# Optimization experiments

Measured on AMD Instinct MI355X. Metric: run time of the kernel, lower is better.

The kernel has to match this reference:

```python
import jax, jax.numpy as jnp
import numpy as np

H = 256  # HIDDEN_SIZE
E = 256  # EMBED_SIZE
B = 128
L = 2048


def setup_inputs() -> dict:
    key = jax.random.key(0)
    ks = jax.random.split(key, 14)
    s = 1.0 / np.sqrt(H)
    return {
        "input_embed": jax.random.normal(ks[0], (B, 1, E), jnp.float32),
        "encoder_outputs": jax.random.normal(ks[1], (B, L, H), jnp.float32),
        "hidden1": jax.random.normal(ks[2], (1, B, H), jnp.float32),
        "cell1": jax.random.normal(ks[3], (1, B, H), jnp.float32),
        "hidden2": jax.random.normal(ks[4], (1, B, H), jnp.float32),
        "cell2": jax.random.normal(ks[5], (1, B, H), jnp.float32),
        "w_ih1": jax.random.normal(ks[6], (4 * H, H), jnp.float32) * s,
        "w_hh1": jax.random.normal(ks[7], (4 * H, H), jnp.float32) * s,
        "b_ih1": jax.random.normal(ks[8], (4 * H,), jnp.float32) * s,
        "b_hh1": jax.random.normal(ks[9], (4 * H,), jnp.float32) * s,
        "w_ih2": jax.random.normal(ks[10], (4 * H, E + H), jnp.float32) * s,
        "w_hh2": jax.random.normal(ks[11], (4 * H, H), jnp.float32) * s,
        "b_ih2": jax.random.normal(ks[12], (4 * H,), jnp.float32) * s,
        "b_hh2": jax.random.normal(ks[13], (4 * H,), jnp.float32) * s,
    }


def _lstm_step(x, h, c, w_ih, w_hh, b_ih, b_hh):
    # x: [B, D_in]; h, c: [B, H]. PyTorch gate order: i, f, g, o.
    gates = x @ w_ih.T + h @ w_hh.T + b_ih + b_hh  # [B, 4H]
    i, f, g, o = jnp.split(gates, 4, axis=-1)
    c_new = jax.nn.sigmoid(f) * c + jax.nn.sigmoid(i) * jnp.tanh(g)
    h_new = jax.nn.sigmoid(o) * jnp.tanh(c_new)
    return h_new, c_new


def reference(input_embed, encoder_outputs, hidden1, cell1, hidden2, cell2,
              w_ih1, w_hh1, b_ih1, b_hh1, w_ih2, w_hh2, b_ih2, b_hh2):
    # Attention: dot-product scores between hidden1[0] and each encoder step.
    scores = jnp.einsum('bh,blh->bl', hidden1[0], encoder_outputs)  # [B, L]
    alpha = jax.nn.softmax(scores, axis=1)
    context = jnp.einsum('bl,blh->bh', alpha, encoder_outputs)  # [B, H]

    # LSTM1 single step on the context vector.
    h1, c1 = _lstm_step(context, hidden1[0], cell1[0], w_ih1, w_hh1, b_ih1, b_hh1)
    mid = h1[:, None, :]  # [B, 1, H]

    # Concat embedding with LSTM1 output, run LSTM2 single step.
    new_mid = jnp.concatenate([input_embed[:, 0, :], h1], axis=-1)  # [B, E+H]
    h2, c2 = _lstm_step(new_mid, hidden2[0], cell2[0], w_ih2, w_hh2, b_ih2, b_hh2)
    outputs = h2[:, None, :]  # [B, 1, H]

    return (outputs, h1[None], c1[None], h2[None], c2[None])
```

## Files before the change

### kernel.cpp

```cpp
#include <hip/hip_runtime.h>
#include <math.h>

#define BN   128
#define LN   2048
#define HN   256
#define EN   256
#define CHUNKS 8
#define ROWS_PER_CHUNK (LN / CHUNKS)
#define PSTRIDE 260

__device__ __forceinline__ float sigmoidf_(float x) { return 1.0f / (1.0f + __expf(-x)); }
__device__ __forceinline__ float tanhf_(float x)    { return 1.0f - 2.0f / (__expf(2.0f * x) + 1.0f); }

__global__ __launch_bounds__(256) void attn_partial(
    const float* __restrict__ enc,
    const float* __restrict__ hidden1,
    float* __restrict__ partials)
{
    const int chunk = blockIdx.x;
    const int b     = blockIdx.y;
    const int t     = threadIdx.x;
    const int wave  = t >> 6;
    const int lane  = t & 63;

    __shared__ float lds_ctx[4][256];
    __shared__ float lds_m[4], lds_s[4];

    const float4 h4 = *(const float4*)(hidden1 + b * HN + lane * 4);

    float  m = -INFINITY, s = 0.0f;
    float4 ctx = make_float4(0.f, 0.f, 0.f, 0.f);

    const float* rowp = enc + ((size_t)b * LN + (size_t)chunk * ROWS_PER_CHUNK + wave * 64) * HN + lane * 4;

    #pragma unroll 2
    for (int r = 0; r < 64; ++r) {
        float4 e = *(const float4*)rowp;
        rowp += HN;
        float d = e.x * h4.x + e.y * h4.y + e.z * h4.z + e.w * h4.w;
        #pragma unroll
        for (int off = 32; off > 0; off >>= 1) d += __shfl_xor(d, off, 64);
        float mn   = fmaxf(m, d);
        float corr = __expf(m - mn);
        float p    = __expf(d - mn);
        s = s * corr + p;
        ctx.x = ctx.x * corr + p * e.x;
        ctx.y = ctx.y * corr + p * e.y;
        ctx.z = ctx.z * corr + p * e.z;
        ctx.w = ctx.w * corr + p * e.w;
        m = mn;
    }

    *(float4*)&lds_ctx[wave][lane * 4] = ctx;
    if (lane == 0) { lds_m[wave] = m; lds_s[wave] = s; }
    __syncthreads();

    float M = fmaxf(fmaxf(lds_m[0], lds_m[1]), fmaxf(lds_m[2], lds_m[3]));
    float e0 = __expf(lds_m[0] - M), e1 = __expf(lds_m[1] - M);
    float e2 = __expf(lds_m[2] - M), e3 = __expf(lds_m[3] - M);
    float cj = e0 * lds_ctx[0][t] + e1 * lds_ctx[1][t] + e2 * lds_ctx[2][t] + e3 * lds_ctx[3][t];
    float S  = e0 * lds_s[0] + e1 * lds_s[1] + e2 * lds_s[2] + e3 * lds_s[3];

    float* pb = partials + ((size_t)b * CHUNKS + chunk) * PSTRIDE;
    pb[t] = cj;
    if (t == 0) { pb[256] = M; pb[257] = S; }
}

#define STAGE_W1(Wp)                                                          \
    {                                                                         \
        _Pragma("unroll")                                                     \
        for (int it = 0; it < 16; ++it) {                                     \
            const int idx = it * 128 + t;                                     \
            const int row = idx & 31;                             \
            const int kf  = idx >> 5;               \
            const int q   = row >> 3, jl0 = row & 7;                          \
            const int g   = q * 256 + jb * 8 + jl0;                           \
            float4 v = *(const float4*)((Wp) + (size_t)g * 256 + kf * 4);     \
            const int pos = ((jl0 ^ (kf & 7)) << 2) + q;                      \
            wq[kf * 128 +  0 + pos] = v.x;                                    \
            wq[kf * 128 + 32 + pos] = v.y;                                    \
            wq[kf * 128 + 64 + pos] = v.z;                                    \
            wq[kf * 128 + 96 + pos] = v.w;                                    \
        }                                                                     \
    }

__global__ __launch_bounds__(128) void lstm1_fused(
    const float* __restrict__ partials,
    const float* __restrict__ hidden1,
    const float* __restrict__ w_ih,
    const float* __restrict__ w_hh,
    const float* __restrict__ b_ih,
    const float* __restrict__ b_hh,
    const float* __restrict__ cell,
    float* __restrict__ h_out,
    float* __restrict__ c_out)
{
    __shared__ float wq[256 * 32];
    __shared__ float xs[16 * 512];
    const int t  = threadIdx.x;
    const int jb = blockIdx.x;
    const int bb = blockIdx.y;

    STAGE_W1(w_ih);

    {
        const int g  = t >> 3;
        const int l8 = t & 7;
        const int b  = bb * 16 + g;
        const float* pb = partials + (size_t)b * CHUNKS * PSTRIDE;

        float mk[CHUNKS], ek[CHUNKS];
        float M = -INFINITY;
        #pragma unroll
        for (int k = 0; k < CHUNKS; ++k) { mk[k] = pb[k * PSTRIDE + 256]; M = fmaxf(M, mk[k]); }
        float S = 0.0f;
        #pragma unroll
        for (int k = 0; k < CHUNKS; ++k) { ek[k] = __expf(mk[k] - M); S += ek[k] * pb[k * PSTRIDE + 257]; }
        const float invS = 1.0f / S;

        #pragma unroll
        for (int it = 0; it < 8; ++it) {
            const int j4 = it * 8 + l8;
            float cx = 0.f, cy = 0.f, cz = 0.f, cw = 0.f;
            #pragma unroll
            for (int k = 0; k < CHUNKS; ++k) {
                float4 p4 = *(const float4*)(pb + k * PSTRIDE + j4 * 4);
                cx += ek[k] * p4.x; cy += ek[k] * p4.y;
                cz += ek[k] * p4.z; cw += ek[k] * p4.w;
            }
            *(float4*)&xs[g * 512 + ((j4 ^ (g & 7)) << 2)] =
                make_float4(cx * invS, cy * invS, cz * invS, cw * invS);
        }
        const float* hr = hidden1 + (size_t)b * HN;
        #pragma unroll
        for (int it = 0; it < 8; ++it) {
            const int j4 = it * 8 + l8;
            float4 hv = *(const float4*)(hr + j4 * 4);
            *(float4*)&xs[g * 512 + (((64 + j4) ^ (g & 7)) << 2)] = hv;
        }
    }
    __syncthreads();

    const int jl = t & 7, bl = t >> 3;
    const int b = bb * 16 + bl;
    const int j = jb * 8 + jl;

    float acc0 = 0.f, acc1 = 0.f, acc2 = 0.f, acc3 = 0.f;

    #pragma unroll 4
    for (int k4 = 0; k4 < 64; ++k4) {
        float4 xv = *(const float4*)&xs[bl * 512 + ((k4 ^ (bl & 7)) << 2)];
        const int pos = (jl ^ (k4 & 7)) << 2;
        #pragma unroll
        for (int i = 0; i < 4; ++i) {
            float xe = (i == 0) ? xv.x : (i == 1) ? xv.y : (i == 2) ? xv.z : xv.w;
            float4 w4 = *(const float4*)&wq[(k4 * 4 + i) * 32 + pos];
            acc0 += w4.x * xe; acc1 += w4.y * xe; acc2 += w4.z * xe; acc3 += w4.w * xe;
        }
    }
    __syncthreads();

    STAGE_W1(w_hh);
    __syncthreads();

    #pragma unroll 4
    for (int k4 = 0; k4 < 64; ++k4) {
        float4 xv = *(const float4*)&xs[bl * 512 + (((64 + k4) ^ (bl & 7)) << 2)];
        const int pos = (jl ^ (k4 & 7)) << 2;
        #pragma unroll
        for (int i = 0; i < 4; ++i) {
            float xe = (i == 0) ? xv.x : (i == 1) ? xv.y : (i == 2) ? xv.z : xv.w;
            float4 w4 = *(const float4*)&wq[(k4 * 4 + i) * 32 + pos];
            acc0 += w4.x * xe; acc1 += w4.y * xe; acc2 += w4.z * xe; acc3 += w4.w * xe;
        }
    }

    float gi = acc0 + b_ih[j]       + b_hh[j];
    float gf = acc1 + b_ih[256 + j] + b_hh[256 + j];
    float gg = acc2 + b_ih[512 + j] + b_hh[512 + j];
    float go = acc3 + b_ih[768 + j] + b_hh[768 + j];

    float cp = cell[b * HN + j];
    float cn = sigmoidf_(gf) * cp + sigmoidf_(gi) * tanhf_(gg);
    float hn = sigmoidf_(go) * tanhf_(cn);

    c_out[b * HN + j] = cn;
    h_out[b * HN + j] = hn;
}

__global__ __launch_bounds__(128) void lstm2_kernel(
    const float* __restrict__ embed,
    const float* __restrict__ h1,
    const float* __restrict__ hidden2,
    const float* __restrict__ w_ih,
    const float* __restrict__ w_hh,
    const float* __restrict__ b_ih,
    const float* __restrict__ b_hh,
    const float* __restrict__ cell,
    float* __restrict__ out0,
    float* __restrict__ h_out,
    float* __restrict__ c_out)
{
    __shared__ float wq[768 * 16];
    const int t  = threadIdx.x;
    const int jb = blockIdx.x;
    const int bb = blockIdx.y;

    #pragma unroll
    for (int it = 0; it < 24; ++it) {
        const int idx = it * 128 + t;
        const int row = idx & 15;
        const int kf  = idx >> 4;
        const int q   = row >> 2, jl0 = row & 3;
        const int g   = q * 256 + jb * 4 + jl0;
        const int k0  = kf * 4;
        const float* src = (k0 < 512) ? (w_ih + (size_t)g * 512 + k0)
                                      : (w_hh + (size_t)g * 256 + (k0 - 512));
        float4 v = *(const float4*)src;
        const int pos = ((jl0 ^ (kf & 3)) << 2) + q;
        wq[kf * 64 +  0 + pos] = v.x;
        wq[kf * 64 + 16 + pos] = v.y;
        wq[kf * 64 + 32 + pos] = v.z;
        wq[kf * 64 + 48 + pos] = v.w;
    }
    __syncthreads();

    const int jl = t & 3, bl = t >> 2;
    const int b = bb * 32 + bl;
    const int j = jb * 4 + jl;

    float acc0 = 0.f, acc1 = 0.f, acc2 = 0.f, acc3 = 0.f;
    const float* xsrc[3] = { embed   + (size_t)b * EN,
                             h1      + (size_t)b * HN,
                             hidden2 + (size_t)b * HN };
    #pragma unroll
    for (int seg = 0; seg < 3; ++seg) {
        const float* xr = xsrc[seg];
        #pragma unroll 4
        for (int k4 = 0; k4 < 64; ++k4) {
            const int kf = seg * 64 + k4;
            float4 xv = *(const float4*)(xr + k4 * 4);
            const int pos = (jl ^ (k4 & 3)) << 2;
            #pragma unroll
            for (int i = 0; i < 4; ++i) {
                float xe = (i == 0) ? xv.x : (i == 1) ? xv.y : (i == 2) ? xv.z : xv.w;
                float4 w4 = *(const float4*)&wq[(kf * 4 + i) * 16 + pos];
                acc0 += w4.x * xe; acc1 += w4.y * xe; acc2 += w4.z * xe; acc3 += w4.w * xe;
            }
        }
    }

    float gi = acc0 + b_ih[j]       + b_hh[j];
    float gf = acc1 + b_ih[256 + j] + b_hh[256 + j];
    float gg = acc2 + b_ih[512 + j] + b_hh[512 + j];
    float go = acc3 + b_ih[768 + j] + b_hh[768 + j];

    float cp = cell[b * HN + j];
    float cn = sigmoidf_(gf) * cp + sigmoidf_(gi) * tanhf_(gg);
    float hn = sigmoidf_(go) * tanhf_(cn);

    out0[b * HN + j]  = hn;
    h_out[b * HN + j] = hn;
    c_out[b * HN + j] = cn;
}

extern "C" void kernel_launch(void* const* d_in, const int* in_sizes, int n_in,
                              void* d_out, int out_size, void* d_ws, size_t ws_size,
                              hipStream_t stream)
{
    const float* embed   = (const float*)d_in[0];
    const float* enc     = (const float*)d_in[1];
    const float* hidden1 = (const float*)d_in[2];
    const float* cell1   = (const float*)d_in[3];
    const float* hidden2 = (const float*)d_in[4];
    const float* cell2   = (const float*)d_in[5];
    const float* w_ih1   = (const float*)d_in[6];
    const float* w_hh1   = (const float*)d_in[7];
    const float* b_ih1   = (const float*)d_in[8];
    const float* b_hh1   = (const float*)d_in[9];
    const float* w_ih2   = (const float*)d_in[10];
    const float* w_hh2   = (const float*)d_in[11];
    const float* b_ih2   = (const float*)d_in[12];
    const float* b_hh2   = (const float*)d_in[13];

    float* out = (float*)d_out;
    float* ws = (float*)d_ws;
    float* partials = ws;

    attn_partial<<<dim3(CHUNKS, BN), 256, 0, stream>>>(enc, hidden1, partials);
    lstm1_fused<<<dim3(32, 8), 128, 0, stream>>>(partials, hidden1, w_ih1, w_hh1,
                                                 b_ih1, b_hh1, cell1,
                                                 out + 32768, out + 65536);
    lstm2_kernel<<<dim3(64, 4), 128, 0, stream>>>(embed, out + 32768, hidden2,
                                                  w_ih2, w_hh2, b_ih2, b_hh2, cell2,
                                                  out, out + 98304, out + 131072);
}
```

Before: 419.1 us.

## Split LSTM K-reduction across two thread halves and stage both weights at once

Both LSTM kernels move to 256 threads per block, and each half of the block accumulates a different part of the K dimension. The halves combine their partial sums through shared memory before the gate nonlinearity. lstm1 now stages w_ih and w_hh together into a doubled LDS buffer, which removes the second staging pass and its barriers. The attention loop unroll goes from 2 to 4. The aim is more parallelism and latency hiding in the small LSTM kernels, at the cost of more LDS per block, which may lower occupancy.

Measured after the change: 410.3 us. -2.1%, faster.

```diff
diff --git a/kernel.cpp b/kernel.cpp
--- a/kernel.cpp
+++ b/kernel.cpp
@@ -33,7 +33,7 @@
 
     const float* rowp = enc + ((size_t)b * LN + (size_t)chunk * ROWS_PER_CHUNK + wave * 64) * HN + lane * 4;
 
-    #pragma unroll 2
+    #pragma unroll 4
     for (int r = 0; r < 64; ++r) {
         float4 e = *(const float4*)rowp;
         rowp += HN;
@@ -66,25 +66,7 @@
     if (t == 0) { pb[256] = M; pb[257] = S; }
 }
 
-#define STAGE_W1(Wp)                                                          \
-    {                                                                         \
-        _Pragma("unroll")                                                     \
-        for (int it = 0; it < 16; ++it) {                                     \
-            const int idx = it * 128 + t;                                     \
-            const int row = idx & 31;                             \
-            const int kf  = idx >> 5;               \
-            const int q   = row >> 3, jl0 = row & 7;                          \
-            const int g   = q * 256 + jb * 8 + jl0;                           \
-            float4 v = *(const float4*)((Wp) + (size_t)g * 256 + kf * 4);     \
-            const int pos = ((jl0 ^ (kf & 7)) << 2) + q;                      \
-            wq[kf * 128 +  0 + pos] = v.x;                                    \
-            wq[kf * 128 + 32 + pos] = v.y;                                    \
-            wq[kf * 128 + 64 + pos] = v.z;                                    \
-            wq[kf * 128 + 96 + pos] = v.w;                                    \
-        }                                                                     \
-    }
-
-__global__ __launch_bounds__(128) void lstm1_fused(
+__global__ __launch_bounds__(256) void lstm1_fused(
     const float* __restrict__ partials,
     const float* __restrict__ hidden1,
     const float* __restrict__ w_ih,
@@ -95,18 +77,36 @@
     float* __restrict__ h_out,
     float* __restrict__ c_out)
 {
-    __shared__ float wq[256 * 32];
+    __shared__ float wq[2 * 256 * 32];
     __shared__ float xs[16 * 512];
+    __shared__ float red[128 * 4];
     const int t  = threadIdx.x;
     const int jb = blockIdx.x;
     const int bb = blockIdx.y;
 
-    STAGE_W1(w_ih);
-
     {
-        const int g  = t >> 3;
-        const int l8 = t & 7;
-        const int b  = bb * 16 + g;
+        const int ri   = t & 63;
+        const int half = ri >> 5;
+        const int row  = ri & 31;
+        const int q = row >> 3, jl0 = row & 7;
+        const int g = q * 256 + jb * 8 + jl0;
+        const float* W = half ? w_hh : w_ih;
+        #pragma unroll
+        for (int it = 0; it < 16; ++it) {
+            const int kf = it * 4 + (t >> 6);
+            float4 v = *(const float4*)(W + (size_t)g * 256 + kf * 4);
+            const int base = half * 8192 + kf * 128 + ((jl0 ^ (kf & 7)) << 2) + q;
+            wq[base +  0] = v.x;
+            wq[base + 32] = v.y;
+            wq[base + 64] = v.z;
+            wq[base + 96] = v.w;
+        }
+    }
+
+    {
+        const int g   = t >> 4;
+        const int l16 = t & 15;
+        const int b   = bb * 16 + g;
         const float* pb = partials + (size_t)b * CHUNKS * PSTRIDE;
 
         float mk[CHUNKS], ek[CHUNKS];
@@ -119,8 +119,8 @@
         const float invS = 1.0f / S;
 
         #pragma unroll
-        for (int it = 0; it < 8; ++it) {
-            const int j4 = it * 8 + l8;
+        for (int it = 0; it < 4; ++it) {
+            const int j4 = it * 16 + l16;
             float cx = 0.f, cy = 0.f, cz = 0.f, cw = 0.f;
             #pragma unroll
             for (int k = 0; k < CHUNKS; ++k) {
@@ -133,62 +133,72 @@
         }
         const float* hr = hidden1 + (size_t)b * HN;
         #pragma unroll
-        for (int it = 0; it < 8; ++it) {
-            const int j4 = it * 8 + l8;
+        for (int it = 0; it < 4; ++it) {
+            const int j4 = it * 16 + l16;
             float4 hv = *(const float4*)(hr + j4 * 4);
             *(float4*)&xs[g * 512 + (((64 + j4) ^ (g & 7)) << 2)] = hv;
         }
     }
     __syncthreads();
 
-    const int jl = t & 7, bl = t >> 3;
+    const int jl = t & 7;
+    const int bl = (t >> 3) & 15;
+    const int kh = t >> 7;
     const int b = bb * 16 + bl;
     const int j = jb * 8 + jl;
 
     float acc0 = 0.f, acc1 = 0.f, acc2 = 0.f, acc3 = 0.f;
-
+    const int xbase = bl * 512;
+    const int wbase = kh * 8192;
     #pragma unroll 4
     for (int k4 = 0; k4 < 64; ++k4) {
-        float4 xv = *(const float4*)&xs[bl * 512 + ((k4 ^ (bl & 7)) << 2)];
+        float4 xv = *(const float4*)&xs[xbase + (((kh << 6) + (k4 ^ (bl & 7))) << 2)];
         const int pos = (jl ^ (k4 & 7)) << 2;
         #pragma unroll
         for (int i = 0; i < 4; ++i) {
             float xe = (i == 0) ? xv.x : (i == 1) ? xv.y : (i == 2) ? xv.z : xv.w;
-            float4 w4 = *(const float4*)&wq[(k4 * 4 + i) * 32 + pos];
+            float4 w4 = *(const float4*)&wq[wbase + (k4 * 4 + i) * 32 + pos];
             acc0 += w4.x * xe; acc1 += w4.y * xe; acc2 += w4.z * xe; acc3 += w4.w * xe;
         }
     }
-    __syncthreads();
-
-    STAGE_W1(w_hh);
-    __syncthreads();
-
-    #pragma unroll 4
-    for (int k4 = 0; k4 < 64; ++k4) {
-        float4 xv = *(const float4*)&xs[bl * 512 + (((64 + k4) ^ (bl & 7)) << 2)];
-        const int pos = (jl ^ (k4 & 7)) << 2;
-        #pragma unroll
-        for (int i = 0; i < 4; ++i) {
-            float xe = (i == 0) ? xv.x : (i == 1) ? xv.y : (i == 2) ? xv.z : xv.w;
-            float4 w4 = *(const float4*)&wq[(k4 * 4 + i) * 32 + pos];
-            acc0 += w4.x * xe; acc1 += w4.y * xe; acc2 += w4.z * xe; acc3 += w4.w * xe;
-        }
-    }
-
-    float gi = acc0 + b_ih[j]       + b_hh[j];
-    float gf = acc1 + b_ih[256 + j] + b_hh[256 + j];
-    float gg = acc2 + b_ih[512 + j] + b_hh[512 + j];
-    float go = acc3 + b_ih[768 + j] + b_hh[768 + j];
-
-    float cp = cell[b * HN + j];
-    float cn = sigmoidf_(gf) * cp + sigmoidf_(gi) * tanhf_(gg);
-    float hn = sigmoidf_(go) * tanhf_(cn);
-
-    c_out[b * HN + j] = cn;
-    h_out[b * HN + j] = hn;
+
+    if (kh == 1) *(float4*)&red[(t - 128) * 4] = make_float4(acc0, acc1, acc2, acc3);
+    __syncthreads();
+
+    if (kh == 0) {
+        float4 r = *(const float4*)&red[t * 4];
+        acc0 += r.x; acc1 += r.y; acc2 += r.z; acc3 += r.w;
+
+        float gi = acc0 + b_ih[j]       + b_hh[j];
+        float gf = acc1 + b_ih[256 + j] + b_hh[256 + j];
+        float gg = acc2 + b_ih[512 + j] + b_hh[512 + j];
+        float go = acc3 + b_ih[768 + j] + b_hh[768 + j];
+
+        float cp = cell[b * HN + j];
+        float cn = sigmoidf_(gf) * cp + sigmoidf_(gi) * tanhf_(gg);
+        float hn = sigmoidf_(go) * tanhf_(cn);
+
+        c_out[b * HN + j] = cn;
+        h_out[b * HN + j] = hn;
+    }
 }
 
-__global__ __launch_bounds__(128) void lstm2_kernel(
+#define DOT2(KF, PTR)                                                         \
+    {                                                                         \
+        float4 xv = *(const float4*)(PTR);                                    \
+        const int pos = (jl ^ ((KF) & 3)) << 2;                               \
+        const float* wp = &wq[(KF) * 64 + pos];                               \
+        float4 w0 = *(const float4*)(wp);                                     \
+        float4 w1 = *(const float4*)(wp + 16);                                \
+        float4 w2 = *(const float4*)(wp + 32);                                \
+        float4 w3 = *(const float4*)(wp + 48);                                \
+        acc0 += w0.x * xv.x + w1.x * xv.y + w2.x * xv.z + w3.x * xv.w;        \
+        acc1 += w0.y * xv.x + w1.y * xv.y + w2.y * xv.z + w3.y * xv.w;        \
+        acc2 += w0.z * xv.x + w1.z * xv.y + w2.z * xv.z + w3.z * xv.w;        \
+        acc3 += w0.w * xv.x + w1.w * xv.y + w2.w * xv.z + w3.w * xv.w;        \
+    }
+
+__global__ __launch_bounds__(256) void lstm2_kernel(
     const float* __restrict__ embed,
     const float* __restrict__ h1,
     const float* __restrict__ hidden2,
@@ -202,13 +212,14 @@
     float* __restrict__ c_out)
 {
     __shared__ float wq[768 * 16];
+    __shared__ float red[128 * 4];
     const int t  = threadIdx.x;
     const int jb = blockIdx.x;
     const int bb = blockIdx.y;
 
     #pragma unroll
-    for (int it = 0; it < 24; ++it) {
-        const int idx = it * 128 + t;
+    for (int it = 0; it < 12; ++it) {
+        const int idx = it * 256 + t;
         const int row = idx & 15;
         const int kf  = idx >> 4;
         const int q   = row >> 2, jl0 = row & 3;
@@ -225,43 +236,50 @@
     }
     __syncthreads();
 
-    const int jl = t & 3, bl = t >> 2;
+    const int jl = t & 3;
+    const int bl = (t >> 2) & 31;
+    const int kh = t >> 7;
     const int b = bb * 32 + bl;
     const int j = jb * 4 + jl;
 
     float acc0 = 0.f, acc1 = 0.f, acc2 = 0.f, acc3 = 0.f;
-    const float* xsrc[3] = { embed   + (size_t)b * EN,
-                             h1      + (size_t)b * HN,
-                             hidden2 + (size_t)b * HN };
-    #pragma unroll
-    for (int seg = 0; seg < 3; ++seg) {
-        const float* xr = xsrc[seg];
+
+    if (kh == 0) {
+        const float* xe_ = embed + (size_t)b * EN;
         #pragma unroll 4
-        for (int k4 = 0; k4 < 64; ++k4) {
-            const int kf = seg * 64 + k4;
-            float4 xv = *(const float4*)(xr + k4 * 4);
-            const int pos = (jl ^ (k4 & 3)) << 2;
-            #pragma unroll
-            for (int i = 0; i < 4; ++i) {
-                float xe = (i == 0) ? xv.x : (i == 1) ? xv.y : (i == 2) ? xv.z : xv.w;
-                float4 w4 = *(const float4*)&wq[(kf * 4 + i) * 16 + pos];
-                acc0 += w4.x * xe; acc1 += w4.y * xe; acc2 += w4.z * xe; acc3 += w4.w * xe;
-            }
-        }
-    }
-
-    float gi = acc0 + b_ih[j]       + b_hh[j];
-    float gf = acc1 + b_ih[256 + j] + b_hh[256 + j];
-    float gg = acc2 + b_ih[512 + j] + b_hh[512 + j];
-    float go = acc3 + b_ih[768 + j] + b_hh[768 + j];
-
-    float cp = cell[b * HN + j];
-    float cn = sigmoidf_(gf) * cp + sigmoidf_(gi) * tanhf_(gg);
-    float hn = sigmoidf_(go) * tanhf_(cn);
-
-    out0[b * HN + j]  = hn;
-    h_out[b * HN + j] = hn;
-    c_out[b * HN + j] = cn;
+        for (int k4 = 0; k4 < 64; ++k4)  DOT2(k4, xe_ + k4 * 4);
+        const float* xh_ = h1 + (size_t)b * HN;
+        #pragma unroll 4
+        for (int k4 = 64; k4 < 96; ++k4) DOT2(k4, xh_ + (k4 - 64) * 4);
+    } else {
+        const float* xh_ = h1 + (size_t)b * HN;
+        #pragma unroll 4
+        for (int k4 = 96; k4 < 128; ++k4)  DOT2(k4, xh_ + (k4 - 64) * 4);
+        const float* xc_ = hidden2 + (size_t)b * HN;
+        #pragma unroll 4
+        for (int k4 = 128; k4 < 192; ++k4) DOT2(k4, xc_ + (k4 - 128) * 4);
+    }
+
+    if (kh == 1) *(float4*)&red[(t - 128) * 4] = make_float4(acc0, acc1, acc2, acc3);
+    __syncthreads();
+
+    if (kh == 0) {
+        float4 r = *(const float4*)&red[t * 4];
+        acc0 += r.x; acc1 += r.y; acc2 += r.z; acc3 += r.w;
+
+        float gi = acc0 + b_ih[j]       + b_hh[j];
+        float gf = acc1 + b_ih[256 + j] + b_hh[256 + j];
+        float gg = acc2 + b_ih[512 + j] + b_hh[512 + j];
+        float go = acc3 + b_ih[768 + j] + b_hh[768 + j];
+
+        float cp = cell[b * HN + j];
+        float cn = sigmoidf_(gf) * cp + sigmoidf_(gi) * tanhf_(gg);
+        float hn = sigmoidf_(go) * tanhf_(cn);
+
+        out0[b * HN + j]  = hn;
+        h_out[b * HN + j] = hn;
+        c_out[b * HN + j] = cn;
+    }
 }
 
 extern "C" void kernel_launch(void* const* d_in, const int* in_sizes, int n_in,
@@ -288,10 +306,10 @@
     float* partials = ws;
 
     attn_partial<<<dim3(CHUNKS, BN), 256, 0, stream>>>(enc, hidden1, partials);
-    lstm1_fused<<<dim3(32, 8), 128, 0, stream>>>(partials, hidden1, w_ih1, w_hh1,
+    lstm1_fused<<<dim3(32, 8), 256, 0, stream>>>(partials, hidden1, w_ih1, w_hh1,
                                                  b_ih1, b_hh1, cell1,
                                                  out + 32768, out + 65536);
-    lstm2_kernel<<<dim3(64, 4), 128, 0, stream>>>(embed, out + 32768, hidden2,
+    lstm2_kernel<<<dim3(64, 4), 256, 0, stream>>>(embed, out + 32768, hidden2,
                                                   w_ih2, w_hh2, b_ih2, b_hh2, cell2,
                                                   out, out + 98304, out + 131072);
 }
```
